# Optimization experiments

Measured on AMD Instinct MI355X. Metric: run time of the kernel, lower is better.

Reference implementation:

```python
import jax, jax.numpy as jnp
import numpy as np

B, S, D = 8, 1024, 1024
H, KV, HD = 16, 16, 64
NDIM = 2
EPS = 1e-6


def rms_norm(x, weight=None, eps=EPS):
    var = jnp.mean(jnp.square(x), axis=-1, keepdims=True)
    out = x * jax.lax.rsqrt(var + eps)
    if weight is not None:
        out = out * weight
    return out


def rotate_half(x):
    half = x.shape[-1] // 2
    return jnp.concatenate((-x[..., half:], x[..., :half]), axis=-1)


def multidim_rope(x, cos, sin, ndim):
    # x: [B,S,H,HD]; cos,sin: [B,S,HD]; head_dim split into ndim contiguous
    # chunks of size per = 2*(HD // (2*ndim)); rotate-half applied per chunk.
    b, s, h, hd = x.shape
    per = 2 * (hd // (2 * ndim))
    xg = x.reshape(b, s, h, ndim, per)
    cg = cos.reshape(b, s, 1, ndim, per)
    sg = sin.reshape(b, s, 1, ndim, per)
    out = xg * cg + rotate_half(xg) * sg
    return out.reshape(b, s, h, hd)


def setup_inputs() -> dict:
    key = jax.random.key(0)
    ks = jax.random.split(key, 10)
    scale = 1.0 / np.sqrt(D)
    return {
        "hidden_states": jax.random.normal(ks[0], (B, S, D), jnp.float32),
        "cos": jax.random.uniform(ks[1], (B, S, HD), jnp.float32, -1.0, 1.0),
        "sin": jax.random.uniform(ks[2], (B, S, HD), jnp.float32, -1.0, 1.0),
        "position_ids": jax.random.randint(ks[3], (B, S, NDIM), 0, 32, jnp.int32),
        "wq": jax.random.normal(ks[4], (D, H * HD), jnp.float32) * scale,
        "wk": jax.random.normal(ks[5], (D, KV * HD), jnp.float32) * scale,
        "wv": jax.random.normal(ks[6], (D, KV * HD), jnp.float32) * scale,
        "wo": jax.random.normal(ks[7], (H * HD, D), jnp.float32) * scale,
        "q_norm_w": jnp.ones((HD,), jnp.float32),
        "k_norm_w": jnp.ones((HD,), jnp.float32),
    }


def reference(hidden_states, cos, sin, position_ids, wq, wk, wv, wo, q_norm_w, k_norm_w):
    b, s, _ = hidden_states.shape
    ndim = position_ids.shape[-1]

    q = (hidden_states @ wq).reshape(b, s, H, HD)
    q = rms_norm(q, q_norm_w)
    q = multidim_rope(q, cos, sin, ndim)

    k = (hidden_states @ wk).reshape(b, s, KV, HD)
    k = rms_norm(k, k_norm_w)
    k = multidim_rope(k, cos, sin, ndim)

    v = (hidden_states @ wv).reshape(b, s, KV, HD)
    v = rms_norm(v, None)  # v_norm has no weight

    # Full (non-causal) vision attention, scaling = 1.0
    scores = jnp.einsum("bqhd,bkhd->bhqk", q, k)
    probs = jax.nn.softmax(scores, axis=-1)
    attn = jnp.einsum("bhqk,bkhd->bqhd", probs, v).reshape(b, s, H * HD)

    return attn @ wo
```

## Files before the change

### kernel.cpp

```cpp
#include <hip/hip_runtime.h>
#include <hip/hip_bf16.h>

typedef __attribute__((ext_vector_type(8))) short bf16x8;
typedef __attribute__((ext_vector_type(4))) short bf16x4;
typedef __attribute__((ext_vector_type(4))) float f32x4;

struct __align__(16) V16 { unsigned long long a, b; };

__device__ __forceinline__ float bf2f(unsigned short u) {
  union { unsigned int i; float f; } c; c.i = ((unsigned int)u) << 16; return c.f;
}
__device__ __forceinline__ unsigned short f2bf(float f) {
  unsigned int u; __builtin_memcpy(&u, &f, 4);
  u += 0x7FFFu + ((u >> 16) & 1u);
  return (unsigned short)(u >> 16);
}

__device__ __forceinline__ void async16(unsigned short* lds,
                                        const unsigned short* g) {
  __builtin_amdgcn_global_load_lds(
      (const __attribute__((address_space(1))) unsigned int*)g,
      (__attribute__((address_space(3))) unsigned int*)lds, 16, 0, 0);
}

#define FP32_MAGIC 0x3F800000u

__device__ __forceinline__ void cvt_seg(
    const void* __restrict__ src, unsigned short* __restrict__ dst,
    int n4, int i, int stride, bool f32)
{
  if (f32) {
    const float* s = (const float*)src;
    for (; i < n4; i += stride) {
      float4 v = *(const float4*)(s + (size_t)i * 4);
      ushort2 lo = { f2bf(v.x), f2bf(v.y) };
      ushort2 hi = { f2bf(v.z), f2bf(v.w) };
      *(ushort2*)(dst + (size_t)i * 4)     = lo;
      *(ushort2*)(dst + (size_t)i * 4 + 2) = hi;
    }
  } else {
    const unsigned short* s = (const unsigned short*)src;
    for (; i < n4; i += stride)
      *(ushort4*)(dst + (size_t)i * 4) = *(const ushort4*)(s + (size_t)i * 4);
  }
}

__global__ __launch_bounds__(256) void cvt_bf16(
    const void* __restrict__ src, size_t srcOff,
    unsigned short* __restrict__ dst, int n4,
    const unsigned int* __restrict__ fmt)
{
  const bool f32 = (fmt[0] == FP32_MAGIC);
  const int i = blockIdx.x * blockDim.x + threadIdx.x;
  const int stride = gridDim.x * blockDim.x;
  const void* s = f32 ? (const void*)((const float*)src + srcOff)
                      : (const void*)((const unsigned short*)src + srcOff);
  cvt_seg(s, dst, n4, i, stride, f32);
}

__global__ __launch_bounds__(256) void cvt_all(
    const void* __restrict__ hid, const void* __restrict__ cosr,
    const void* __restrict__ sinr, const void* __restrict__ qnw,
    const void* __restrict__ knw,
    unsigned short* __restrict__ hb, unsigned short* __restrict__ csb,
    unsigned short* __restrict__ snb, unsigned short* __restrict__ qnb,
    unsigned short* __restrict__ knb,
    int hidden_n4, const unsigned int* __restrict__ fmt)
{
  const bool f32 = (fmt[0] == FP32_MAGIC);
  const int bx = blockIdx.x, tid = threadIdx.x;
  if (bx < 2048) {
    if (hidden_n4 > 0)
      cvt_seg(hid, hb, hidden_n4, bx * 256 + tid, 2048 * 256, f32);
  } else if (bx < 2176) {
    cvt_seg(cosr, csb, 131072, (bx - 2048) * 256 + tid, 128 * 256, f32);
  } else if (bx < 2304) {
    cvt_seg(sinr, snb, 131072, (bx - 2176) * 256 + tid, 128 * 256, f32);
  } else {
    if (tid < 16)       cvt_seg(qnw, qnb, 16, tid, 16, f32);
    else if (tid < 32)  cvt_seg(knw, knb, 16, tid - 16, 16, f32);
  }
}

__global__ __launch_bounds__(256) void cvt_t4(
    const void* __restrict__ s0, const void* __restrict__ s1,
    const void* __restrict__ s2, const void* __restrict__ s3,
    unsigned short* __restrict__ d0, unsigned short* __restrict__ d1,
    unsigned short* __restrict__ d2, unsigned short* __restrict__ d3,
    const unsigned int* __restrict__ fmt)
{
  __shared__ __align__(16) unsigned short T[64][72];
  const int z = blockIdx.z;
  const void* src = (z == 0) ? s0 : (z == 1) ? s1 : (z == 2) ? s2 : s3;
  unsigned short* dstT = (z == 0) ? d0 : (z == 1) ? d1 : (z == 2) ? d2 : d3;

  const bool f32 = (fmt[0] == FP32_MAGIC);
  const int tid = threadIdx.x;
  const int k0 = blockIdx.x * 64, n0 = blockIdx.y * 64;
  const int rl = tid >> 3, cl = (tid & 7) * 8;

#pragma unroll
  for (int p = 0; p < 2; ++p) {
    int r = rl + p * 32;
    int cs = cl ^ (r & 56);
    if (f32) {
      const float* s = (const float*)src + (size_t)(k0 + r) * 1024 + n0 + cl;
      float4 v0 = *(const float4*)s, v1 = *(const float4*)(s + 4);
      unsigned short* t = &T[r][cs];
      t[0]=f2bf(v0.x); t[1]=f2bf(v0.y); t[2]=f2bf(v0.z); t[3]=f2bf(v0.w);
      t[4]=f2bf(v1.x); t[5]=f2bf(v1.y); t[6]=f2bf(v1.z); t[7]=f2bf(v1.w);
    } else {
      *(V16*)&T[r][cs] = *(const V16*)((const unsigned short*)src +
                                        (size_t)(k0 + r) * 1024 + n0 + cl);
    }
  }
  __syncthreads();

#pragma unroll
  for (int p = 0; p < 2; ++p) {
    int u = tid + p * 256;
    int d = u >> 3, sc = (u & 7) * 8;
    unsigned short tmp[8];
#pragma unroll
    for (int i = 0; i < 8; ++i) tmp[i] = T[sc + i][d ^ sc];
    *(V16*)&dstT[(size_t)(n0 + d) * 1024 + k0 + sc] = *(V16*)tmp;
  }
}

__global__ __launch_bounds__(256) void transpose_v(
    const unsigned short* __restrict__ v, unsigned short* __restrict__ vt)
{
  __shared__ __align__(16) unsigned short T[64][72];
  const int tid = threadIdx.x;
  const int s0 = blockIdx.x * 64;
  const int bh = blockIdx.y;
  const int b = bh >> 4, h = bh & 15;
  const int rl = tid >> 3, cl = (tid & 7) * 8;

#pragma unroll
  for (int p = 0; p < 2; ++p) {
    int r = rl + p * 32;
    *(V16*)&T[r][cl ^ (r & 56)] = *(const V16*)(
        v + (size_t)(b * 1024 + s0 + r) * 1024 + h * 64 + cl);
  }
  __syncthreads();

#pragma unroll
  for (int p = 0; p < 2; ++p) {
    int u = tid + p * 256;
    int d = u >> 3, sc = (u & 7) * 8;
    unsigned short tmp[8];
#pragma unroll
    for (int i = 0; i < 8; ++i) tmp[i] = T[sc + i][d ^ sc];
    *(V16*)&vt[(size_t)(bh * 64 + d) * 1024 + s0 + sc] = *(V16*)tmp;
  }
}

#define TM 128
#define TN 128
#define TK 64
#define GK 1024

__global__ __launch_bounds__(256) void gemm_qkv(
    const unsigned short* __restrict__ A,
    const unsigned short* __restrict__ Bt,
    unsigned short* __restrict__ Cq,
    unsigned short* __restrict__ Ck,
    unsigned short* __restrict__ Cv,
    const unsigned short* __restrict__ cs,
    const unsigned short* __restrict__ sn,
    const unsigned short* __restrict__ qw,
    const unsigned short* __restrict__ kw,
    int M)
{
  __shared__ __align__(16) unsigned short As[TM][TK];
  __shared__ __align__(16) unsigned short Bs[TN][TK];

  const int tid  = threadIdx.x;
  const int wave = tid >> 6;
  const int lane = tid & 63;
  const int quad = lane >> 4;
  const int l16  = lane & 15;
  const int bm = blockIdx.x * TM;
  const int bn = blockIdx.y * TN;
  const int wm = (wave & 1) * 64;
  const int wn = (wave >> 1) * 64;

  const f32x4 z = {0.f, 0.f, 0.f, 0.f};
  f32x4 acc[4][4];
#pragma unroll
  for (int i = 0; i < 4; ++i)
#pragma unroll
    for (int j = 0; j < 4; ++j) acc[i][j] = z;

  const int lrow = lane >> 3;
  const int gcol = ((lane & 7) ^ lrow) * 8;
  const unsigned short* aP = A  + (size_t)(bm + wave * 8 + lrow) * GK + gcol;
  const unsigned short* bP = Bt + (size_t)(bn + wave * 8 + lrow) * GK + gcol;
  const int cswz = l16 & 7;

  for (int k0 = 0; k0 < GK; k0 += TK) {
#pragma unroll
    for (int p = 0; p < 4; ++p) {
      async16(&As[p * 32 + wave * 8][0], aP + (size_t)p * 32 * GK);
      async16(&Bs[p * 32 + wave * 8][0], bP + (size_t)p * 32 * GK);
    }
    aP += TK; bP += TK;
    __syncthreads();

#pragma unroll
    for (int s = 0; s < 2; ++s) {
      const int pc = ((s * 4 + quad) ^ cswz) * 8;
      bf16x8 af[4], bfv[4];
#pragma unroll
      for (int mt = 0; mt < 4; ++mt)
        af[mt] = *(const bf16x8*)&As[wm + mt * 16 + l16][pc];
#pragma unroll
      for (int nt = 0; nt < 4; ++nt)
        bfv[nt] = *(const bf16x8*)&Bs[wn + nt * 16 + l16][pc];
#pragma unroll
      for (int mt = 0; mt < 4; ++mt)
#pragma unroll
        for (int nt = 0; nt < 4; ++nt)
          acc[mt][nt] = __builtin_amdgcn_mfma_f32_16x16x32_bf16(
              af[mt], bfv[nt], acc[mt][nt], 0, 0, 0);
    }
    __syncthreads();
  }

  const int which = bn >> 10;
  unsigned short* Cd = (which == 0) ? Cq : (which == 1) ? Ck : Cv;
  const int colbase = (bn & 1023) + wn;

  float wgt[4];
#pragma unroll
  for (int nt = 0; nt < 4; ++nt) {
    int d = nt * 16 + l16;
    wgt[nt] = (which == 0) ? bf2f(qw[d]) * 1.44269504f
            : (which == 1) ? bf2f(kw[d]) : 1.f;
  }

#pragma unroll
  for (int mt = 0; mt < 4; ++mt)
#pragma unroll
    for (int r = 0; r < 4; ++r) {
      const int row = bm + wm + mt * 16 + quad * 4 + r;
      float x0 = acc[mt][0][r], x1 = acc[mt][1][r];
      float x2 = acc[mt][2][r], x3 = acc[mt][3][r];
      float ss = x0 * x0 + x1 * x1 + x2 * x2 + x3 * x3;
      ss += __shfl_xor(ss, 1);
      ss += __shfl_xor(ss, 2);
      ss += __shfl_xor(ss, 4);
      ss += __shfl_xor(ss, 8);
      const float inv = rsqrtf(ss * (1.f / 64.f) + 1e-6f);
      float y[4] = { x0 * inv * wgt[0], x1 * inv * wgt[1],
                     x2 * inv * wgt[2], x3 * inv * wgt[3] };
      float outv[4];
      if (which < 2) {
        const unsigned short* cp = cs + (size_t)row * 64 + l16;
        const unsigned short* sp = sn + (size_t)row * 64 + l16;
#pragma unroll
        for (int nt = 0; nt < 4; ++nt) {
          float c = bf2f(cp[nt * 16]), s = bf2f(sp[nt * 16]);
          float part = (nt & 1) ? y[nt ^ 1] : -y[nt ^ 1];
          outv[nt] = y[nt] * c + part * s;
        }
      } else {
#pragma unroll
        for (int nt = 0; nt < 4; ++nt) outv[nt] = y[nt];
      }
#pragma unroll
      for (int nt = 0; nt < 4; ++nt)
        Cd[(size_t)row * 1024 + colbase + nt * 16 + l16] = f2bf(outv[nt]);
    }
}

__global__ __launch_bounds__(256) void gemm_bf16(
    const unsigned short* __restrict__ A,
    const unsigned short* __restrict__ Bt,
    void* __restrict__ C, size_t cOff,
    const unsigned int* __restrict__ outFmt,
    int M, int N)
{
  __shared__ __align__(16) unsigned short As[TM][TK];
  __shared__ __align__(16) unsigned short Bs[TN][TK];

  const int tid  = threadIdx.x;
  const int wave = tid >> 6;
  const int lane = tid & 63;
  const int quad = lane >> 4;
  const int l16  = lane & 15;
  const int bm = blockIdx.x * TM;
  const int bn = blockIdx.y * TN;
  const int wm = (wave & 1) * 64;
  const int wn = (wave >> 1) * 64;

  const f32x4 z = {0.f, 0.f, 0.f, 0.f};
  f32x4 acc[4][4];
#pragma unroll
  for (int i = 0; i < 4; ++i)
#pragma unroll
    for (int j = 0; j < 4; ++j) acc[i][j] = z;

  const int lrow = lane >> 3;
  const int gcol = ((lane & 7) ^ lrow) * 8;
  const unsigned short* aP = A  + (size_t)(bm + wave * 8 + lrow) * GK + gcol;
  const unsigned short* bP = Bt + (size_t)(bn + wave * 8 + lrow) * GK + gcol;
  const int cswz = l16 & 7;

  for (int k0 = 0; k0 < GK; k0 += TK) {
#pragma unroll
    for (int p = 0; p < 4; ++p) {
      async16(&As[p * 32 + wave * 8][0], aP + (size_t)p * 32 * GK);
      async16(&Bs[p * 32 + wave * 8][0], bP + (size_t)p * 32 * GK);
    }
    aP += TK; bP += TK;
    __syncthreads();

#pragma unroll
    for (int s = 0; s < 2; ++s) {
      const int pc = ((s * 4 + quad) ^ cswz) * 8;
      bf16x8 af[4], bfv[4];
#pragma unroll
      for (int mt = 0; mt < 4; ++mt)
        af[mt] = *(const bf16x8*)&As[wm + mt * 16 + l16][pc];
#pragma unroll
      for (int nt = 0; nt < 4; ++nt)
        bfv[nt] = *(const bf16x8*)&Bs[wn + nt * 16 + l16][pc];
#pragma unroll
      for (int mt = 0; mt < 4; ++mt)
#pragma unroll
        for (int nt = 0; nt < 4; ++nt)
          acc[mt][nt] = __builtin_amdgcn_mfma_f32_16x16x32_bf16(
              af[mt], bfv[nt], acc[mt][nt], 0, 0, 0);
    }
    __syncthreads();
  }

  const bool of32 = (outFmt != nullptr) && (outFmt[0] == FP32_MAGIC);
  float* Cf = (float*)C + cOff;
  unsigned short* Ch = (unsigned short*)C + cOff;

#pragma unroll
  for (int mt = 0; mt < 4; ++mt)
#pragma unroll
    for (int nt = 0; nt < 4; ++nt)
#pragma unroll
      for (int r = 0; r < 4; ++r) {
        int row = bm + wm + mt * 16 + quad * 4 + r;
        int col = bn + wn + nt * 16 + l16;
        size_t idx = (size_t)row * N + col;
        if (of32) Cf[idx] = acc[mt][nt][r];
        else      Ch[idx] = f2bf(acc[mt][nt][r]);
      }
}

__global__ __launch_bounds__(256) void attn_fused(
    const unsigned short* __restrict__ q,
    const unsigned short* __restrict__ k,
    const unsigned short* __restrict__ vt,
    unsigned short* __restrict__ o)
{
  __shared__ __align__(16) unsigned short Ks[2][64][64];
  __shared__ __align__(16) unsigned short Vs[2][64][64];

  const int tid  = threadIdx.x;
  const int wave = tid >> 6;
  const int lane = tid & 63;
  const int quad = lane >> 4;
  const int l16  = lane & 15;
  const int bh = blockIdx.y;
  const int b  = bh >> 4, h = bh & 15;
  const int qbase = blockIdx.x * 64 + wave * 16;
  const size_t bbase = (size_t)b * 1024;

  bf16x8 qf[2];
  {
    const unsigned short* qp = q + (bbase + qbase + l16) * 1024 + h * 64;
    qf[0] = *(const bf16x8*)(qp + quad * 8);
    qf[1] = *(const bf16x8*)(qp + 32 + quad * 8);
  }

  const f32x4 z = {0.f, 0.f, 0.f, 0.f};
  f32x4 of[5];
#pragma unroll
  for (int nt = 0; nt < 5; ++nt) of[nt] = z;
  float m_run = -1e30f;

  const bf16x8 onesv = { 0x3F80, 0x3F80, 0x3F80, 0x3F80,
                         0x3F80, 0x3F80, 0x3F80, 0x3F80 };

  const int lrow = lane >> 3;
  const int gcol = ((lane & 7) ^ lrow) * 8;
  const unsigned short* kP = k  + (bbase + wave * 8 + lrow) * 1024 + h * 64 + gcol;
  const unsigned short* vP = vt + ((size_t)bh * 64 + wave * 8 + lrow) * 1024 + gcol;
  const int cswz = l16 & 7;

  auto STAGE = [&](int buf, int kt) {
#pragma unroll
    for (int p = 0; p < 2; ++p) {
      async16(&Ks[buf][p * 32 + wave * 8][0], kP + ((size_t)kt * 64 + p * 32) * 1024);
      async16(&Vs[buf][p * 32 + wave * 8][0], vP + (size_t)p * 32 * 1024 + kt * 64);
    }
  };

  STAGE(0, 0);
  __syncthreads();

#pragma unroll 2
  for (int kt = 0; kt < 16; ++kt) {
    const int cur = kt & 1;
    if (kt < 15) STAGE(cur ^ 1, kt + 1);

    f32x4 sf[4];
#pragma unroll
    for (int nt = 0; nt < 4; ++nt) sf[nt] = z;
    __builtin_amdgcn_s_setprio(1);
#pragma unroll
    for (int s = 0; s < 2; ++s) {
      const int pc = ((s * 4 + quad) ^ cswz) * 8;
#pragma unroll
      for (int nt = 0; nt < 4; ++nt) {
        bf16x8 kf = *(const bf16x8*)&Ks[cur][nt * 16 + l16][pc];
        sf[nt] = __builtin_amdgcn_mfma_f32_16x16x32_bf16(kf, qf[s], sf[nt], 0, 0, 0);
      }
    }
    __builtin_amdgcn_s_setprio(0);

    float m0 = fmaxf(fmaxf(sf[0][0], sf[0][1]), fmaxf(sf[0][2], sf[0][3]));
    float m1 = fmaxf(fmaxf(sf[1][0], sf[1][1]), fmaxf(sf[1][2], sf[1][3]));
    float m2 = fmaxf(fmaxf(sf[2][0], sf[2][1]), fmaxf(sf[2][2], sf[2][3]));
    float m3 = fmaxf(fmaxf(sf[3][0], sf[3][1]), fmaxf(sf[3][2], sf[3][3]));
    float mx = fmaxf(fmaxf(m0, m1), fmaxf(m2, m3));
    mx = fmaxf(mx, __shfl_xor(mx, 16));
    mx = fmaxf(mx, __shfl_xor(mx, 32));

    if (!__all(mx - m_run <= 11.5f)) {
      float mn = fmaxf(m_run, mx);
      float alpha = __builtin_amdgcn_exp2f(m_run - mn);
      m_run = mn;
      float ar[4];
#pragma unroll
      for (int r = 0; r < 4; ++r) ar[r] = __shfl(alpha, quad * 4 + r);
#pragma unroll
      for (int nt = 0; nt < 5; ++nt)
#pragma unroll
        for (int r = 0; r < 4; ++r) of[nt][r] *= ar[r];
    }

    union PFU { bf16x8 v; unsigned int w[4]; } pfu[2];
#pragma unroll
    for (int nt = 0; nt < 4; ++nt) {
      float e0 = __builtin_amdgcn_exp2f(sf[nt][0] - m_run);
      float e1 = __builtin_amdgcn_exp2f(sf[nt][1] - m_run);
      float e2 = __builtin_amdgcn_exp2f(sf[nt][2] - m_run);
      float e3 = __builtin_amdgcn_exp2f(sf[nt][3] - m_run);
      unsigned int w0, w1;
      asm("v_cvt_pk_bf16_f32 %0, %1, %2" : "=v"(w0) : "v"(e0), "v"(e1));
      asm("v_cvt_pk_bf16_f32 %0, %1, %2" : "=v"(w1) : "v"(e2), "v"(e3));
      pfu[nt >> 1].w[(nt & 1) * 2]     = w0;
      pfu[nt >> 1].w[(nt & 1) * 2 + 1] = w1;
    }

    __builtin_amdgcn_s_setprio(1);
#pragma unroll
    for (int s = 0; s < 2; ++s) {
#pragma unroll
      for (int nt = 0; nt < 4; ++nt) {
        const unsigned short* vrow = &Vs[cur][nt * 16 + l16][0];
        const int g0  = (4 * s + (quad >> 1)) ^ cswz;
        const int off = 4 * (quad & 1);
        bf16x4 v0 = *(const bf16x4*)(vrow + g0 * 8 + off);
        bf16x4 v1 = *(const bf16x4*)(vrow + (g0 ^ 2) * 8 + off);
        bf16x8 vf = __builtin_shufflevector(v0, v1, 0, 1, 2, 3, 4, 5, 6, 7);
        of[nt] = __builtin_amdgcn_mfma_f32_16x16x32_bf16(pfu[s].v, vf, of[nt], 0, 0, 0);
      }
      of[4] = __builtin_amdgcn_mfma_f32_16x16x32_bf16(pfu[s].v, onesv, of[4], 0, 0, 0);
    }
    __builtin_amdgcn_s_setprio(0);

    __syncthreads();
  }

  float invl[4];
#pragma unroll
  for (int r = 0; r < 4; ++r) invl[r] = 1.f / of[4][r];
#pragma unroll
  for (int nt = 0; nt < 4; ++nt)
#pragma unroll
    for (int r = 0; r < 4; ++r) {
      int row = qbase + quad * 4 + r;
      o[(bbase + row) * 1024 + h * 64 + nt * 16 + l16] = f2bf(of[nt][r] * invl[r]);
    }
}

extern "C" void kernel_launch(void* const* d_in, const int* in_sizes, int n_in,
                              void* d_out, int out_size, void* d_ws, size_t ws_size,
                              hipStream_t stream) {
  const void* hidden = d_in[0];
  const void* cosr   = d_in[1];
  const void* sinr   = d_in[2];
  const void* wq     = d_in[4];
  const void* wk     = d_in[5];
  const void* wv     = d_in[6];
  const void* wo     = d_in[7];
  const void* qnw    = d_in[8];
  const void* knw    = d_in[9];
  const unsigned int* fmt = (const unsigned int*)qnw;

  const size_t MEG = 1024 * 1024;
  dim3 blk(256);
  unsigned short* w = (unsigned short*)d_ws;

  if (ws_size >= (size_t)60 * MEG) {
    unsigned short* hb   = w;
    unsigned short* vtb  = w;
    unsigned short* wqT  = w + 8 * MEG;
    unsigned short* wkT  = w + 9 * MEG;
    unsigned short* wvT  = w + 10 * MEG;
    unsigned short* woT  = w + 11 * MEG;
    unsigned short* csb  = w + 12 * MEG;
    unsigned short* snb  = w + 12 * MEG + 512 * 1024;
    unsigned short* qnb  = w + 13 * MEG;
    unsigned short* knb  = w + 13 * MEG + 64;
    unsigned short* qb   = w + 14 * MEG;
    unsigned short* kb   = w + 22 * MEG;
    unsigned short* vb   = (unsigned short*)d_out;
    unsigned short* ab   = qb;

    cvt_all<<<dim3(2305), blk, 0, stream>>>(hidden, cosr, sinr, qnw, knw,
                                            hb, csb, snb, qnb, knb,
                                            2 * (int)MEG, fmt);
    cvt_t4<<<dim3(16, 16, 4), blk, 0, stream>>>(wq, wk, wv, wo,
                                                wqT, wkT, wvT, woT, fmt);

    const int M = 8192;
    gemm_qkv<<<dim3(M / TM, 24), blk, 0, stream>>>(hb, wqT, qb, kb, vb,
                                                   csb, snb, qnb, knb, M);
    transpose_v<<<dim3(16, 8 * 16), blk, 0, stream>>>(vb, vtb);
    attn_fused<<<dim3(16, 8 * 16), blk, 0, stream>>>(qb, kb, vtb, ab);
    gemm_bf16<<<dim3(M / TM, 8), blk, 0, stream>>>(ab, woT, d_out, 0, fmt,
                                                   M, 1024);
  } else {
    unsigned short* wqT  = w;
    unsigned short* wkT  = w + 1 * MEG;
    unsigned short* wvT  = w + 2 * MEG;
    unsigned short* woT  = w + 3 * MEG;
    unsigned short* csb  = w + 4 * MEG;
    unsigned short* snb  = w + 4 * MEG + 512 * 1024;
    unsigned short* qnb  = w + 5 * MEG;
    unsigned short* knb  = w + 5 * MEG + 64;
    unsigned short* hbb  = w + 6 * MEG;
    unsigned short* qb   = w + 7 * MEG;
    unsigned short* kb   = w + 8 * MEG;
    unsigned short* vb   = w + 9 * MEG;
    unsigned short* vtb  = w + 10 * MEG;

    cvt_t4<<<dim3(16, 16, 4), blk, 0, stream>>>(wq, wk, wv, wo,
                                                wqT, wkT, wvT, woT, fmt);
    cvt_all<<<dim3(2305), blk, 0, stream>>>(hidden, cosr, sinr, qnw, knw,
                                            nullptr, csb, snb, qnb, knb,
                                            0, fmt);

    const int Mb = 1024;
    for (int b = 0; b < 8; ++b) {
      cvt_bf16<<<dim3(512), blk, 0, stream>>>(hidden, (size_t)b * MEG, hbb,
                                              (int)(MEG / 4), fmt);
      gemm_qkv<<<dim3(Mb / TM, 24), blk, 0, stream>>>(
          hbb, wqT, qb, kb, vb, csb + (size_t)b * 64 * 1024,
          snb + (size_t)b * 64 * 1024, qnb, knb, Mb);
      transpose_v<<<dim3(16, 16), blk, 0, stream>>>(vb, vtb);
      attn_fused<<<dim3(16, 16), blk, 0, stream>>>(qb, kb, vtb, qb);
      gemm_bf16<<<dim3(Mb / TM, 8), blk, 0, stream>>>(qb, woT, d_out,
                                                      (size_t)b * MEG, fmt,
                                                      Mb, 1024);
    }
  }
}
```

Baseline: 279.4 us.

## Fuse V transpose into QKV GEMM epilogue via per-wave LDS staging

```diff
diff --git a/kernel.cpp b/kernel.cpp
--- a/kernel.cpp
+++ b/kernel.cpp
@@ -127,35 +127,6 @@
   }
 }
 
-__global__ __launch_bounds__(256) void transpose_v(
-    const unsigned short* __restrict__ v, unsigned short* __restrict__ vt)
-{
-  __shared__ __align__(16) unsigned short T[64][72];
-  const int tid = threadIdx.x;
-  const int s0 = blockIdx.x * 64;
-  const int bh = blockIdx.y;
-  const int b = bh >> 4, h = bh & 15;
-  const int rl = tid >> 3, cl = (tid & 7) * 8;
-
-#pragma unroll
-  for (int p = 0; p < 2; ++p) {
-    int r = rl + p * 32;
-    *(V16*)&T[r][cl ^ (r & 56)] = *(const V16*)(
-        v + (size_t)(b * 1024 + s0 + r) * 1024 + h * 64 + cl);
-  }
-  __syncthreads();
-
-#pragma unroll
-  for (int p = 0; p < 2; ++p) {
-    int u = tid + p * 256;
-    int d = u >> 3, sc = (u & 7) * 8;
-    unsigned short tmp[8];
-#pragma unroll
-    for (int i = 0; i < 8; ++i) tmp[i] = T[sc + i][d ^ sc];
-    *(V16*)&vt[(size_t)(bh * 64 + d) * 1024 + s0 + sc] = *(V16*)tmp;
-  }
-}
-
 #define TM 128
 #define TN 128
 #define TK 64
@@ -173,8 +144,9 @@
     const unsigned short* __restrict__ kw,
     int M)
 {
-  __shared__ __align__(16) unsigned short As[TM][TK];
-  __shared__ __align__(16) unsigned short Bs[TN][TK];
+  __shared__ __align__(16) unsigned short LDSu[2 * TM * TK];
+  unsigned short (*As)[TK] = (unsigned short (*)[TK])LDSu;
+  unsigned short (*Bs)[TK] = (unsigned short (*)[TK])&LDSu[TM * TK];
 
   const int tid  = threadIdx.x;
   const int wave = tid >> 6;
@@ -229,15 +201,52 @@
   }
 
   const int which = bn >> 10;
-  unsigned short* Cd = (which == 0) ? Cq : (which == 1) ? Ck : Cv;
   const int colbase = (bn & 1023) + wn;
 
+  if (which == 2) {
+    unsigned short* Tw = LDSu + wave * 4096;
+#pragma unroll
+    for (int mt = 0; mt < 4; ++mt)
+#pragma unroll
+      for (int r = 0; r < 4; ++r) {
+        const int s = mt * 16 + quad * 4 + r;
+        float x0 = acc[mt][0][r], x1 = acc[mt][1][r];
+        float x2 = acc[mt][2][r], x3 = acc[mt][3][r];
+        float ss = x0 * x0 + x1 * x1 + x2 * x2 + x3 * x3;
+        ss += __shfl_xor(ss, 1);
+        ss += __shfl_xor(ss, 2);
+        ss += __shfl_xor(ss, 4);
+        ss += __shfl_xor(ss, 8);
+        const float inv = rsqrtf(ss * (1.f / 64.f) + 1e-6f);
+        const int sw = (s >> 3) << 3;
+#pragma unroll
+        for (int nt = 0; nt < 4; ++nt)
+          Tw[s * 64 + ((nt * 16 + l16) ^ sw)] = f2bf(acc[mt][nt][r] * inv);
+      }
+    __builtin_amdgcn_wave_barrier();
+
+    const int vhead = ((bm >> 10) * 16 + (colbase >> 6)) * 64;
+    const int sbase = (bm & 1023) + wm;
+    const int sg = (lane & 7) * 8;
+    const int dl = lane >> 3;
+#pragma unroll
+    for (int p = 0; p < 8; ++p) {
+      const int d = p * 8 + dl;
+      unsigned short tmp[8];
+#pragma unroll
+      for (int i = 0; i < 8; ++i)
+        tmp[i] = Tw[(sg + i) * 64 + (d ^ sg)];
+      *(V16*)&Cv[(size_t)(vhead + d) * 1024 + sbase + sg] = *(V16*)tmp;
+    }
+    return;
+  }
+
+  unsigned short* Cd = (which == 0) ? Cq : Ck;
   float wgt[4];
 #pragma unroll
   for (int nt = 0; nt < 4; ++nt) {
     int d = nt * 16 + l16;
-    wgt[nt] = (which == 0) ? bf2f(qw[d]) * 1.44269504f
-            : (which == 1) ? bf2f(kw[d]) : 1.f;
+    wgt[nt] = (which == 0) ? bf2f(qw[d]) * 1.44269504f : bf2f(kw[d]);
   }
 
 #pragma unroll
@@ -255,23 +264,15 @@
       const float inv = rsqrtf(ss * (1.f / 64.f) + 1e-6f);
       float y[4] = { x0 * inv * wgt[0], x1 * inv * wgt[1],
                      x2 * inv * wgt[2], x3 * inv * wgt[3] };
-      float outv[4];
-      if (which < 2) {
-        const unsigned short* cp = cs + (size_t)row * 64 + l16;
-        const unsigned short* sp = sn + (size_t)row * 64 + l16;
-#pragma unroll
-        for (int nt = 0; nt < 4; ++nt) {
-          float c = bf2f(cp[nt * 16]), s = bf2f(sp[nt * 16]);
-          float part = (nt & 1) ? y[nt ^ 1] : -y[nt ^ 1];
-          outv[nt] = y[nt] * c + part * s;
-        }
-      } else {
-#pragma unroll
-        for (int nt = 0; nt < 4; ++nt) outv[nt] = y[nt];
+      const unsigned short* cp = cs + (size_t)row * 64 + l16;
+      const unsigned short* sp = sn + (size_t)row * 64 + l16;
+#pragma unroll
+      for (int nt = 0; nt < 4; ++nt) {
+        float c = bf2f(cp[nt * 16]), s = bf2f(sp[nt * 16]);
+        float part = (nt & 1) ? y[nt ^ 1] : -y[nt ^ 1];
+        Cd[(size_t)row * 1024 + colbase + nt * 16 + l16] =
+            f2bf(y[nt] * c + part * s);
       }
-#pragma unroll
-      for (int nt = 0; nt < 4; ++nt)
-        Cd[(size_t)row * 1024 + colbase + nt * 16 + l16] = f2bf(outv[nt]);
     }
 }
 
@@ -448,19 +449,13 @@
         for (int r = 0; r < 4; ++r) of[nt][r] *= ar[r];
     }
 
-    union PFU { bf16x8 v; unsigned int w[4]; } pfu[2];
-#pragma unroll
-    for (int nt = 0; nt < 4; ++nt) {
-      float e0 = __builtin_amdgcn_exp2f(sf[nt][0] - m_run);
-      float e1 = __builtin_amdgcn_exp2f(sf[nt][1] - m_run);
-      float e2 = __builtin_amdgcn_exp2f(sf[nt][2] - m_run);
-      float e3 = __builtin_amdgcn_exp2f(sf[nt][3] - m_run);
-      unsigned int w0, w1;
-      asm("v_cvt_pk_bf16_f32 %0, %1, %2" : "=v"(w0) : "v"(e0), "v"(e1));
-      asm("v_cvt_pk_bf16_f32 %0, %1, %2" : "=v"(w1) : "v"(e2), "v"(e3));
-      pfu[nt >> 1].w[(nt & 1) * 2]     = w0;
-      pfu[nt >> 1].w[(nt & 1) * 2 + 1] = w1;
-    }
+    bf16x8 pf[2];
+#pragma unroll
+    for (int nt = 0; nt < 4; ++nt)
+#pragma unroll
+      for (int r = 0; r < 4; ++r)
+        pf[nt >> 1][(nt & 1) * 4 + r] =
+            (short)f2bf(__builtin_amdgcn_exp2f(sf[nt][r] - m_run));
 
     __builtin_amdgcn_s_setprio(1);
 #pragma unroll
@@ -473,9 +468,9 @@
         bf16x4 v0 = *(const bf16x4*)(vrow + g0 * 8 + off);
         bf16x4 v1 = *(const bf16x4*)(vrow + (g0 ^ 2) * 8 + off);
         bf16x8 vf = __builtin_shufflevector(v0, v1, 0, 1, 2, 3, 4, 5, 6, 7);
-        of[nt] = __builtin_amdgcn_mfma_f32_16x16x32_bf16(pfu[s].v, vf, of[nt], 0, 0, 0);
+        of[nt] = __builtin_amdgcn_mfma_f32_16x16x32_bf16(pf[s], vf, of[nt], 0, 0, 0);
       }
-      of[4] = __builtin_amdgcn_mfma_f32_16x16x32_bf16(pfu[s].v, onesv, of[4], 0, 0, 0);
+      of[4] = __builtin_amdgcn_mfma_f32_16x16x32_bf16(pf[s], onesv, of[4], 0, 0, 0);
     }
     __builtin_amdgcn_s_setprio(0);
 
@@ -514,7 +509,6 @@
 
   if (ws_size >= (size_t)60 * MEG) {
     unsigned short* hb   = w;
-    unsigned short* vtb  = w;
     unsigned short* wqT  = w + 8 * MEG;
     unsigned short* wkT  = w + 9 * MEG;
     unsigned short* wvT  = w + 10 * MEG;
@@ -525,7 +519,7 @@
     unsigned short* knb  = w + 13 * MEG + 64;
     unsigned short* qb   = w + 14 * MEG;
     unsigned short* kb   = w + 22 * MEG;
-    unsigned short* vb   = (unsigned short*)d_out;
+    unsigned short* vtb  = (unsigned short*)d_out;
     unsigned short* ab   = qb;
 
     cvt_all<<<dim3(2305), blk, 0, stream>>>(hidden, cosr, sinr, qnw, knw,
@@ -535,9 +529,8 @@
                                                 wqT, wkT, wvT, woT, fmt);
 
     const int M = 8192;
-    gemm_qkv<<<dim3(M / TM, 24), blk, 0, stream>>>(hb, wqT, qb, kb, vb,
+    gemm_qkv<<<dim3(M / TM, 24), blk, 0, stream>>>(hb, wqT, qb, kb, vtb,
                                                    csb, snb, qnb, knb, M);
-    transpose_v<<<dim3(16, 8 * 16), blk, 0, stream>>>(vb, vtb);
     attn_fused<<<dim3(16, 8 * 16), blk, 0, stream>>>(qb, kb, vtb, ab);
     gemm_bf16<<<dim3(M / TM, 8), blk, 0, stream>>>(ab, woT, d_out, 0, fmt,
                                                    M, 1024);
@@ -553,7 +546,6 @@
     unsigned short* hbb  = w + 6 * MEG;
     unsigned short* qb   = w + 7 * MEG;
     unsigned short* kb   = w + 8 * MEG;
-    unsigned short* vb   = w + 9 * MEG;
     unsigned short* vtb  = w + 10 * MEG;
 
     cvt_t4<<<dim3(16, 16, 4), blk, 0, stream>>>(wq, wk, wv, wo,
@@ -567,9 +559,8 @@
       cvt_bf16<<<dim3(512), blk, 0, stream>>>(hidden, (size_t)b * MEG, hbb,
                                               (int)(MEG / 4), fmt);
       gemm_qkv<<<dim3(Mb / TM, 24), blk, 0, stream>>>(
-          hbb, wqT, qb, kb, vb, csb + (size_t)b * 64 * 1024,
+          hbb, wqT, qb, kb, vtb, csb + (size_t)b * 64 * 1024,
           snb + (size_t)b * 64 * 1024, qnb, knb, Mb);
-      transpose_v<<<dim3(16, 16), blk, 0, stream>>>(vb, vtb);
       attn_fused<<<dim3(16, 16), blk, 0, stream>>>(qb, kb, vtb, qb);
       gemm_bf16<<<dim3(Mb / TM, 8), blk, 0, stream>>>(qb, woT, d_out,
                                                       (size_t)b * MEG, fmt,
```

Result: faster. 270.8 us (-3.1%).
